# Kernel optimization log

Hardware: AMD Instinct MI355X
Metric: run time of the kernel (lower is better)

## Reference

```python
import jax, jax.numpy as jnp
import numpy as np

N = 50000
E = 600000
IN_DIM = 128
HID = 128
HEADS = 4
OUT = HID // HEADS  # per-head out channels
R = 2
LAYERS = 2
NEG_SLOPE = 0.2


def _glorot(key, shape):
    fan_in, fan_out = shape[-2], shape[-1]
    lim = jnp.sqrt(6.0 / (fan_in + fan_out))
    return jax.random.uniform(key, shape, jnp.float32, -lim, lim)


def setup_inputs() -> dict:
    key = jax.random.key(0)
    ks = jax.random.split(key, 20)
    x = jax.random.normal(ks[0], (N, IN_DIM), jnp.float32)
    eidx = jax.random.randint(ks[1], (2, E), 0, N, jnp.int64 if jax.config.jax_enable_x64 else jnp.int32)
    etype = jax.random.randint(ks[2], (E,), 0, R, eidx.dtype)
    d = IN_DIM
    params = {}
    ki = 3
    for l in range(LAYERS):
        params[f"W{l}"] = _glorot(ks[ki], (R, d, HID)); ki += 1            # per-relation weight
        params[f"Q{l}"] = _glorot(ks[ki], (HID, HEADS)); ki += 1           # query proj (dim=1)
        params[f"K{l}"] = _glorot(ks[ki], (HID, HEADS)); ki += 1           # key proj
        params[f"cb{l}"] = jnp.zeros((HID,), jnp.float32)                   # conv bias
        params[f"pW{l}"] = _glorot(ks[ki], (HID, HID)); ki += 1            # proj Linear weight [out,in]
        params[f"pb{l}"] = jnp.zeros((HID,), jnp.float32)
        d = HID
    return dict(x=x, eidx=eidx, etype=etype, **params)


def _rgat_conv(h, src, dst, etype, W, Q, K, b):
    # per-relation transform of all nodes: [R, N, HID]
    xw = jnp.einsum('ni,rio->rno', h, W)
    out_j = xw[etype, src]          # [E, HID] source features under edge's relation
    out_i = xw[etype, dst]          # [E, HID] target features under edge's relation
    # additive self-attention, dim=1: alpha [E, HEADS]
    alpha = jax.nn.leaky_relu(out_i @ Q + out_j @ K, NEG_SLOPE)
    # segment softmax over destination nodes (across-relation)
    m = jax.ops.segment_max(alpha, dst, num_segments=N)
    m = jnp.where(jnp.isfinite(m), m, 0.0)
    e = jnp.exp(alpha - m[dst])
    s = jax.ops.segment_sum(e, dst, num_segments=N)
    a = e / (s[dst] + 1e-16)
    # weighted messages and scatter-sum aggregation
    msg = out_j.reshape(E, HEADS, OUT) * a[:, :, None]
    agg = jax.ops.segment_sum(msg.reshape(E, HID), dst, num_segments=N)
    return agg + b


def reference(x, eidx, etype, W0, Q0, K0, cb0, pW0, pb0, W1, Q1, K1, cb1, pW1, pb1):
    src, dst = eidx[0], eidx[1]  # flow source_to_target: aggregate at eidx[1]
    h = x
    for (W, Q, K, cb, pW, pb) in ((W0, Q0, K0, cb0, pW0, pb0), (W1, Q1, K1, cb1, pW1, pb1)):
        h = _rgat_conv(h, src, dst, etype, W, Q, K, cb)
        h = jax.nn.elu(h @ pW.T + pb)
    return h
```

## Files before the change

### kernel.cpp

```cpp
#include <hip/hip_runtime.h>
#include <hip/hip_bf16.h>

typedef __hip_bfloat16 bf16;
typedef short s16x8 __attribute__((ext_vector_type(8)));
typedef float f32x4 __attribute__((ext_vector_type(4)));

#define N_NODES 50000
#define NPAD    50048
#define E_EDGES 600000
#define HID     128
#define HEADS   4
#define SCAN_B  196

__device__ __forceinline__ unsigned short f2bf_bits(float f) {
  unsigned u = __float_as_uint(f);
  u += 0x7fffu + ((u >> 16) & 1u);
  return (unsigned short)(u >> 16);
}
__device__ __forceinline__ float bf2f(unsigned short b) {
  return __uint_as_float(((unsigned)b) << 16);
}
__device__ __forceinline__ float lo_f(unsigned v) { return __uint_as_float(v << 16); }
__device__ __forceinline__ float hi_f(unsigned v) { return __uint_as_float(v & 0xffff0000u); }

__device__ __forceinline__ float lrelu(float v) { return fmaxf(v, 0.2f * v); }

__global__ __launch_bounds__(256) void detect_zero_kernel(const unsigned short* __restrict__ xb,
                                                          const int* __restrict__ ei,
                                                          int* __restrict__ flags,
                                                          int* __restrict__ zp, int nz) {
  int t = threadIdx.x;
  int i = blockIdx.x * 256 + t;
  if (i < nz) zp[i] = 0;
  if (blockIdx.x == 0) {
    __shared__ int cnt[2];
    if (t < 2) cnt[t] = 0;
    __syncthreads();
    unsigned short v = xb[2 * t];
    int ex = (v >> 7) & 0xFF;
    if (ex < 119 || ex > 135) atomicAdd(&cnt[0], 1);
    if (ei[2 * t + 1] != 0) atomicAdd(&cnt[1], 1);
    __syncthreads();
    if (t == 0) {
      flags[0] = (cnt[0] > 64) ? 1 : 0;
      flags[1] = (cnt[1] == 0) ? 1 : 0;
    }
  }
}

__global__ __launch_bounds__(256) void cvt_idx_hist_kernel(const int* __restrict__ eidx,
                                                           const int* __restrict__ etype,
                                                           int* __restrict__ dstA, int* __restrict__ pk,
                                                           int* __restrict__ deg,
                                                           const int* __restrict__ flags) {
  int e = blockIdx.x * 256 + threadIdx.x;
  if (e >= E_EDGES) return;
  int s, d, r;
  if (flags[1]) {
    const long long* e64 = (const long long*)eidx;
    const long long* t64 = (const long long*)etype;
    s = (int)e64[e]; d = (int)e64[E_EDGES + e]; r = (int)t64[e];
  } else {
    s = eidx[e]; d = eidx[E_EDGES + e]; r = etype[e];
  }
  dstA[e] = d;
  pk[e] = s | (r << 16);
  atomicAdd(&deg[d], 1);
}

__global__ __launch_bounds__(256) void cvt_xb_kernel(const void* __restrict__ src,
                                                     unsigned short* __restrict__ dst, int n8,
                                                     const int* __restrict__ flags) {
  int i = blockIdx.x * 256 + threadIdx.x;
  if (i >= n8) return;
  if (flags[0]) {
    const float4* s4 = (const float4*)src;
    float4 a = s4[2 * i], b = s4[2 * i + 1];
    s16x8 o;
    o[0] = (short)f2bf_bits(a.x); o[1] = (short)f2bf_bits(a.y);
    o[2] = (short)f2bf_bits(a.z); o[3] = (short)f2bf_bits(a.w);
    o[4] = (short)f2bf_bits(b.x); o[5] = (short)f2bf_bits(b.y);
    o[6] = (short)f2bf_bits(b.z); o[7] = (short)f2bf_bits(b.w);
    *(s16x8*)(dst + (size_t)i * 8) = o;
  } else {
    *(s16x8*)(dst + (size_t)i * 8) = ((const s16x8*)src)[i];
  }
}

__global__ __launch_bounds__(256) void cvt_wt_kernel(const void* __restrict__ src0,
                                                     const void* __restrict__ src1,
                                                     unsigned short* __restrict__ dst,
                                                     const int* __restrict__ flags) {
  int idx = blockIdx.x * 256 + threadIdx.x;
  if (idx >= 2 * 2 * HID * HID) return;
  int l = idx >> 15, rem = idx & 32767;
  int r = rem >> 14, i = (rem >> 7) & 127, o = rem & 127;
  const void* src = l ? src1 : src0;
  unsigned short b;
  if (flags[0]) b = f2bf_bits(((const float*)src)[rem]);
  else          b = ((const unsigned short*)src)[rem];
  dst[(size_t)l * 2 * HID * HID + ((size_t)r * HID + o) * HID + i] = b;
}

struct P8 { const void* src[8]; int dstoff[8]; int n[8]; };
__global__ __launch_bounds__(256) void cvt_params_kernel(P8 tab, float* __restrict__ base,
                                                         const int* __restrict__ flags) {
  const int f = flags[0];
  for (int k = 0; k < 8; ++k) {
    int n = tab.n[k];
    for (int i = blockIdx.x * 256 + threadIdx.x; i < n; i += gridDim.x * 256) {
      float v = f ? ((const float*)tab.src[k])[i] : bf2f(((const unsigned short*)tab.src[k])[i]);
      base[tab.dstoff[k] + i] = v;
    }
  }
}

__global__ __launch_bounds__(256) void scan1_kernel(const int* __restrict__ deg,
                                                    int* __restrict__ excl,
                                                    int* __restrict__ bsum) {
  __shared__ int sm[256];
  int t = threadIdx.x, i = blockIdx.x * 256 + t;
  int v = (i < NPAD) ? deg[i] : 0;
  sm[t] = v;
  __syncthreads();
#pragma unroll
  for (int off = 1; off < 256; off <<= 1) {
    int add = (t >= off) ? sm[t - off] : 0;
    __syncthreads();
    sm[t] += add;
    __syncthreads();
  }
  if (i < NPAD) excl[i] = sm[t] - v;
  if (t == 255) bsum[blockIdx.x] = sm[255];
}

__global__ __launch_bounds__(256) void scan23_kernel(const int* __restrict__ excl,
                                                     const int* __restrict__ bsum,
                                                     int* __restrict__ rowstart) {
  __shared__ int sm[256];
  int t = threadIdx.x;
  int v = (t < SCAN_B) ? bsum[t] : 0;
  sm[t] = v;
  __syncthreads();
#pragma unroll
  for (int off = 1; off < 256; off <<= 1) {
    int add = (t >= off) ? sm[t - off] : 0;
    __syncthreads();
    sm[t] += add;
    __syncthreads();
  }
  int bpre = (blockIdx.x > 0) ? sm[blockIdx.x - 1] : 0;
  int i = blockIdx.x * 256 + t;
  if (i < NPAD) rowstart[i] = excl[i] + bpre;
  if (i == 0) rowstart[NPAD] = E_EDGES;
}

__global__ __launch_bounds__(256) void scatter_kernel(const int* __restrict__ dstA,
                                                      const int* __restrict__ pk,
                                                      const int* __restrict__ rowstart,
                                                      int* __restrict__ cnt,
                                                      int* __restrict__ eord) {
  int e = blockIdx.x * 256 + threadIdx.x;
  if (e >= E_EDGES) return;
  int d = dstA[e];
  int pos = rowstart[d] + atomicAdd(&cnt[d], 1);
  eord[pos] = pk[e];
}


__global__ __launch_bounds__(256) void gemm_xw_mfma(const unsigned short* __restrict__ hb,
                                                    const unsigned short* __restrict__ Wbt,
                                                    unsigned short* __restrict__ xw) {
  __shared__ unsigned short As[64][136];
  const int t = threadIdx.x;
  const int wave = t >> 6, lane = t & 63;
  const int row0 = blockIdx.x * 64;
  const int r = wave >> 1, colb = (wave & 1) * 64;
  const int lm = lane & 15, q = lane >> 4;
  const unsigned short* Bt = Wbt + (size_t)r * HID * HID;
  s16x8 bfr[4][4];
#pragma unroll
  for (int kc = 0; kc < 4; ++kc) {
    const int ko = kc * 32 + q * 8;
#pragma unroll
    for (int ct = 0; ct < 4; ++ct)
      bfr[kc][ct] = *(const s16x8*)(Bt + (size_t)(colb + ct * 16 + lm) * HID + ko);
  }
  const unsigned short* gsrc = hb + (size_t)row0 * HID;
#pragma unroll
  for (int j = 0; j < 4; ++j) {
    int idx = j * 256 + t;
    *(s16x8*)&As[idx >> 4][(idx & 15) * 8] = *(const s16x8*)(gsrc + idx * 8);
  }
  __syncthreads();
  f32x4 acc[4][4];
#pragma unroll
  for (int a = 0; a < 4; ++a)
#pragma unroll
    for (int b = 0; b < 4; ++b) { f32x4 z = {0.f, 0.f, 0.f, 0.f}; acc[a][b] = z; }
#pragma unroll
  for (int kc = 0; kc < 4; ++kc) {
    const int ko = kc * 32 + q * 8;
#pragma unroll
    for (int rt = 0; rt < 4; ++rt) {
      s16x8 a = *(const s16x8*)&As[rt * 16 + lm][ko];
#pragma unroll
      for (int ct = 0; ct < 4; ++ct)
        acc[rt][ct] = __builtin_amdgcn_mfma_f32_16x16x32_bf16(a, bfr[kc][ct], acc[rt][ct], 0, 0, 0);
    }
  }
  __syncthreads();
#pragma unroll
  for (int rr = 0; rr < 2; ++rr) {
    if (r == rr) {
#pragma unroll
      for (int rt = 0; rt < 4; ++rt)
#pragma unroll
        for (int i = 0; i < 4; ++i) {
          int rloc = rt * 16 + q * 4 + i;
#pragma unroll
          for (int ct = 0; ct < 4; ++ct)
            As[rloc][colb + ct * 16 + lm] = f2bf_bits(acc[rt][ct][i]);
        }
    }
    __syncthreads();
    unsigned short* dst = xw + ((size_t)rr * NPAD + row0) * HID;
#pragma unroll
    for (int j = 0; j < 4; ++j) {
      int idx = j * 256 + t;
      int rw = idx >> 4, cb8 = (idx & 15) * 8;
      if (row0 + rw < N_NODES)
        *(s16x8*)(dst + (size_t)rw * HID + cb8) = *(const s16x8*)&As[rw][cb8];
    }
    __syncthreads();
  }
}

__global__ __launch_bounds__(128) void proj_mfma(const unsigned short* __restrict__ aggb,
                                                 const unsigned short* __restrict__ pWTb,
                                                 const float* __restrict__ bo,
                                                 unsigned short* __restrict__ hbout,
                                                 void* __restrict__ dout,
                                                 const int* __restrict__ flags) {
  __shared__ unsigned short As[64][136];
  const int t = threadIdx.x;
  const int wave = t >> 6, lane = t & 63;
  const int row0 = blockIdx.x * 64;
  const int colb = wave * 64;
  const int lm = lane & 15, q = lane >> 4;
  s16x8 bfr[4][4];
#pragma unroll
  for (int kc = 0; kc < 4; ++kc) {
    const int ko = kc * 32 + q * 8;
#pragma unroll
    for (int ct = 0; ct < 4; ++ct)
      bfr[kc][ct] = *(const s16x8*)(pWTb + (size_t)(colb + ct * 16 + lm) * HID + ko);
  }
  const unsigned short* gsrc = aggb + (size_t)row0 * HID;
#pragma unroll
  for (int j = 0; j < 8; ++j) {
    int idx = j * 128 + t;
    *(s16x8*)&As[idx >> 4][(idx & 15) * 8] = *(const s16x8*)(gsrc + idx * 8);
  }
  __syncthreads();
  f32x4 acc[4][4];
#pragma unroll
  for (int a = 0; a < 4; ++a)
#pragma unroll
    for (int b = 0; b < 4; ++b) { f32x4 z = {0.f, 0.f, 0.f, 0.f}; acc[a][b] = z; }
#pragma unroll
  for (int kc = 0; kc < 4; ++kc) {
    const int ko = kc * 32 + q * 8;
#pragma unroll
    for (int rt = 0; rt < 4; ++rt) {
      s16x8 a = *(const s16x8*)&As[rt * 16 + lm][ko];
#pragma unroll
      for (int ct = 0; ct < 4; ++ct)
        acc[rt][ct] = __builtin_amdgcn_mfma_f32_16x16x32_bf16(a, bfr[kc][ct], acc[rt][ct], 0, 0, 0);
    }
  }
  __syncthreads();
  const int f32final = (dout != nullptr) && flags[0];
  if (!f32final) {
    unsigned short* dstp = dout ? (unsigned short*)dout : hbout;
#pragma unroll
    for (int rt = 0; rt < 4; ++rt)
#pragma unroll
      for (int i = 0; i < 4; ++i) {
        int rloc = rt * 16 + q * 4 + i;
#pragma unroll
        for (int ct = 0; ct < 4; ++ct) {
          int o = colb + ct * 16 + lm;
          float v = acc[rt][ct][i] + bo[o];
          v = v > 0.f ? v : expm1f(v);
          As[rloc][o] = f2bf_bits(v);
        }
      }
    __syncthreads();
#pragma unroll
    for (int j = 0; j < 8; ++j) {
      int idx = j * 128 + t;
      int rw = idx >> 4, cb8 = (idx & 15) * 8;
      if (row0 + rw < N_NODES)
        *(s16x8*)(dstp + (size_t)(row0 + rw) * HID + cb8) = *(const s16x8*)&As[rw][cb8];
    }
  } else {
    float* fdst = (float*)dout;
    float (*Fs)[132] = (float(*)[132])&As[0][0];
#pragma unroll
    for (int h = 0; h < 2; ++h) {
#pragma unroll
      for (int rt2 = 0; rt2 < 2; ++rt2) {
        const int rt = h * 2 + rt2;
#pragma unroll
        for (int i = 0; i < 4; ++i) {
          int rloc = rt2 * 16 + q * 4 + i;
#pragma unroll
          for (int ct = 0; ct < 4; ++ct) {
            int o = colb + ct * 16 + lm;
            float v = acc[rt][ct][i] + bo[o];
            v = v > 0.f ? v : expm1f(v);
            Fs[rloc][o] = v;
          }
        }
      }
      __syncthreads();
#pragma unroll
      for (int j = 0; j < 8; ++j) {
        int idx = j * 128 + t;
        int rw = idx >> 5, cb4 = (idx & 31) * 4;
        if (row0 + h * 32 + rw < N_NODES)
          *(float4*)(fdst + (size_t)(row0 + h * 32 + rw) * HID + cb4) = *(const float4*)&Fs[rw][cb4];
      }
      __syncthreads();
    }
  }
}

__global__ __launch_bounds__(256) void prep_wq_kernel(const unsigned short* __restrict__ Wbt,
                                                      const float* __restrict__ Qf,
                                                      const float* __restrict__ Kf,
                                                      unsigned short* __restrict__ qkt_hi,
                                                      unsigned short* __restrict__ qkt_lo) {
  int idx = blockIdx.x * 256 + threadIdx.x;
  if (idx >= 2 * 2 * HID) return;
  int i = idx & 127, lr = idx >> 7, l = lr >> 1, r = (lr & 1);
  float aq[4] = {0.f, 0.f, 0.f, 0.f}, ak[4] = {0.f, 0.f, 0.f, 0.f};
  const unsigned short* Wb = Wbt + (size_t)lr * HID * HID;
  const float* Qp = Qf + l * HID * HEADS;
  const float* Kp = Kf + l * HID * HEADS;
  for (int j = 0; j < HID; ++j) {
    float w = bf2f(Wb[j * HID + i]);
    float4 q4 = *(const float4*)(Qp + j * 4);
    float4 k4 = *(const float4*)(Kp + j * 4);
    aq[0] += w * q4.x; aq[1] += w * q4.y; aq[2] += w * q4.z; aq[3] += w * q4.w;
    ak[0] += w * k4.x; ak[1] += w * k4.y; ak[2] += w * k4.z; ak[3] += w * k4.w;
  }
  size_t base = (size_t)l * 16 * HID;
#pragma unroll
  for (int h = 0; h < 4; ++h) {
    unsigned short qh = f2bf_bits(aq[h]);
    unsigned short kh = f2bf_bits(ak[h]);
    float qres = aq[h] - bf2f(qh);
    float kres = ak[h] - bf2f(kh);
    qkt_hi[base + (size_t)(r * 4 + h) * HID + i] = qh;
    qkt_lo[base + (size_t)(r * 4 + h) * HID + i] = f2bf_bits(qres);
    qkt_hi[base + (size_t)(8 + r * 4 + h) * HID + i] = kh;
    qkt_lo[base + (size_t)(8 + r * 4 + h) * HID + i] = f2bf_bits(kres);
  }
}

__global__ __launch_bounds__(256) void qk_mfma_kernel(const unsigned short* __restrict__ hb,
                                                      const unsigned short* __restrict__ qkt_hi,
                                                      const unsigned short* __restrict__ qkt_lo,
                                                      float4* __restrict__ qi4,
                                                      float4* __restrict__ kj4) {
  __shared__ float st[4][16][68];
  const int wave = threadIdx.x >> 6, lane = threadIdx.x & 63;
  const int row0 = blockIdx.x * 256 + wave * 64;
  const int lm = lane & 15, q = lane >> 4;
  if (row0 < NPAD) {
    s16x8 bhi[4], blo[4], af[4][4];
#pragma unroll
    for (int kc = 0; kc < 4; ++kc) {
      const int ko = kc * 32 + q * 8;
      bhi[kc] = *(const s16x8*)(qkt_hi + (size_t)lm * HID + ko);
      blo[kc] = *(const s16x8*)(qkt_lo + (size_t)lm * HID + ko);
    }
#pragma unroll
    for (int kc = 0; kc < 4; ++kc) {
      const int ko = kc * 32 + q * 8;
#pragma unroll
      for (int rt = 0; rt < 4; ++rt)
        af[kc][rt] = *(const s16x8*)(hb + (size_t)(row0 + rt * 16 + lm) * HID + ko);
    }
    f32x4 acc[4];
#pragma unroll
    for (int a = 0; a < 4; ++a) { f32x4 z = {0.f, 0.f, 0.f, 0.f}; acc[a] = z; }
#pragma unroll
    for (int kc = 0; kc < 4; ++kc)
#pragma unroll
      for (int rt = 0; rt < 4; ++rt) {
        acc[rt] = __builtin_amdgcn_mfma_f32_16x16x32_bf16(af[kc][rt], bhi[kc], acc[rt], 0, 0, 0);
        acc[rt] = __builtin_amdgcn_mfma_f32_16x16x32_bf16(af[kc][rt], blo[kc], acc[rt], 0, 0, 0);
      }
#pragma unroll
    for (int rt = 0; rt < 4; ++rt)
      *(f32x4*)&st[wave][lm][rt * 16 + q * 4] = acc[rt];
  }
  __syncthreads();
  if (row0 < NPAD) {
    int n = row0 + lane;
    if (n < N_NODES) {
      float4 v;
      v.x = st[wave][0][lane]; v.y = st[wave][1][lane]; v.z = st[wave][2][lane]; v.w = st[wave][3][lane];
      qi4[n] = v;
      v.x = st[wave][4][lane]; v.y = st[wave][5][lane]; v.z = st[wave][6][lane]; v.w = st[wave][7][lane];
      qi4[NPAD + n] = v;
      v.x = st[wave][8][lane]; v.y = st[wave][9][lane]; v.z = st[wave][10][lane]; v.w = st[wave][11][lane];
      kj4[n] = v;
      v.x = st[wave][12][lane]; v.y = st[wave][13][lane]; v.z = st[wave][14][lane]; v.w = st[wave][15][lane];
      kj4[NPAD + n] = v;
    }
  }
}

__global__ __launch_bounds__(256) void edge_fused_kernel(
    const int* __restrict__ rowstart, const int* __restrict__ eord,
    const float4* __restrict__ qi4, const float4* __restrict__ kj4,
    const unsigned short* __restrict__ xw, unsigned short* __restrict__ aggb) {
  __shared__ volatile float wls[4][4][72];
  const int wave = threadIdx.x >> 6, lane = threadIdx.x & 63;
  const int n = blockIdx.x * 4 + wave;
  unsigned* outp = (unsigned*)(aggb + ((size_t)n << 7)) + lane;
  const int start = rowstart[n];
  const int deg = rowstart[n + 1] - start;
  if (deg == 0) { *outp = 0u; return; }
  const int hh = lane >> 4;
  const int ch2 = lane << 1;
  float2 acc = {0.f, 0.f};
  float ssel;
  if (deg <= 64) {
    int p = 0;
    float w0 = 0.f, w1 = 0.f, w2 = 0.f, w3 = 0.f;
    if (lane < deg) {
      p = eord[start + lane];
      int s = p & 0xffff, r = p >> 16;
      float4 k4 = kj4[r ? (NPAD + s) : s];
      float4 q4 = r ? qi4[NPAD + n] : qi4[n];
      w0 = __expf(fminf(lrelu(q4.x + k4.x), 85.f));
      w1 = __expf(fminf(lrelu(q4.y + k4.y), 85.f));
      w2 = __expf(fminf(lrelu(q4.z + k4.z), 85.f));
      w3 = __expf(fminf(lrelu(q4.w + k4.w), 85.f));
    }
    float s0 = w0, s1 = w1, s2 = w2, s3 = w3;
#pragma unroll
    for (int off = 32; off > 0; off >>= 1) {
      s0 += __shfl_xor(s0, off); s1 += __shfl_xor(s1, off);
      s2 += __shfl_xor(s2, off); s3 += __shfl_xor(s3, off);
    }
    ssel = hh == 0 ? s0 : hh == 1 ? s1 : hh == 2 ? s2 : s3;
    wls[wave][0][lane] = w0;
    wls[wave][1][lane] = w1;
    wls[wave][2][lane] = w2;
    wls[wave][3][lane] = w3;
    volatile const float* wrh = &wls[wave][hh][0];
    const int degp = (deg + 15) & ~15;
#pragma unroll 1
    for (int e = 0; e < degp; e += 16) {
      int pp[16];
      unsigned vv[16];
#pragma unroll
      for (int u = 0; u < 16; ++u)
        pp[u] = __builtin_amdgcn_readlane(p, e + u);
#pragma unroll
      for (int u = 0; u < 16; ++u)
        vv[u] = *(const unsigned*)(xw + ((size_t)((pp[u] & 0xffff) + (pp[u] >> 16) * NPAD) << 7) + ch2);
#pragma unroll
      for (int u = 0; u < 16; ++u) {
        float we = wrh[e + u];
        acc.x = fmaf(lo_f(vv[u]), we, acc.x);
        acc.y = fmaf(hi_f(vv[u]), we, acc.y);
      }
    }
  } else {
    const float4 q0 = qi4[n], q1 = qi4[NPAD + n];
    float4 m = make_float4(-1e30f, -1e30f, -1e30f, -1e30f);
    for (int e = start; e < start + deg; ++e) {
      int pe = eord[e];
      int s = pe & 0xffff, r = pe >> 16;
      float4 k4 = kj4[(size_t)r * NPAD + s];
      float4 q4 = r ? q1 : q0;
      m.x = fmaxf(m.x, lrelu(q4.x + k4.x)); m.y = fmaxf(m.y, lrelu(q4.y + k4.y));
      m.z = fmaxf(m.z, lrelu(q4.z + k4.z)); m.w = fmaxf(m.w, lrelu(q4.w + k4.w));
    }
    float4 sv = make_float4(0.f, 0.f, 0.f, 0.f);
    for (int e = start; e < start + deg; ++e) {
      int pe = eord[e];
      int s = pe & 0xffff, r = pe >> 16;
      float4 k4 = kj4[(size_t)r * NPAD + s];
      float4 q4 = r ? q1 : q0;
      float w0 = __expf(lrelu(q4.x + k4.x) - m.x);
      float w1 = __expf(lrelu(q4.y + k4.y) - m.y);
      float w2 = __expf(lrelu(q4.z + k4.z) - m.z);
      float w3 = __expf(lrelu(q4.w + k4.w) - m.w);
      sv.x += w0; sv.y += w1; sv.z += w2; sv.w += w3;
      float we = hh == 0 ? w0 : hh == 1 ? w1 : hh == 2 ? w2 : w3;
      unsigned v = *(const unsigned*)(xw + (((size_t)r * NPAD + s) << 7) + ch2);
      acc.x = fmaf(lo_f(v), we, acc.x);
      acc.y = fmaf(hi_f(v), we, acc.y);
    }
    ssel = hh == 0 ? sv.x : hh == 1 ? sv.y : hh == 2 ? sv.z : sv.w;
  }
  float inv = 1.f / (ssel + 1e-16f);
  *outp = (unsigned)f2bf_bits(acc.x * inv) | ((unsigned)f2bf_bits(acc.y * inv) << 16);
}

__global__ __launch_bounds__(64) void prep_proj_kernel(const void* __restrict__ pW0,
                                                       const void* __restrict__ pW1,
                                                       const float* __restrict__ cbf,
                                                       const float* __restrict__ pbf,
                                                       unsigned short* __restrict__ pWTb2,
                                                       float* __restrict__ bo2,
                                                       const int* __restrict__ flags) {
  int o = blockIdx.x & 127, l = blockIdx.x >> 7, t = threadIdx.x;
  const void* pWraw = l ? pW1 : pW0;
  const float* cb = cbf + l * HID;
  const int f = flags[0];
  float part = 0.f;
#pragma unroll
  for (int i = t; i < HID; i += 64) {
    float w = f ? ((const float*)pWraw)[o * HID + i] : bf2f(((const unsigned short*)pWraw)[o * HID + i]);
    pWTb2[(size_t)l * HID * HID + o * HID + i] = f2bf_bits(w);
    part += cb[i] * w;
  }
#pragma unroll
  for (int off = 32; off > 0; off >>= 1) part += __shfl_xor(part, off);
  if (t == 0) bo2[l * HID + o] = pbf[l * HID + o] + part;
}

extern "C" void kernel_launch(void* const* d_in, const int* in_sizes, int n_in,
                              void* d_out, int out_size, void* d_ws, size_t ws_size,
                              hipStream_t stream) {
  const void* x     = d_in[0];
  const int*  eidx  = (const int*)d_in[1];
  const int*  etype = (const int*)d_in[2];
  const int iW[2] = {3, 9}, iQ[2] = {4, 10}, iK[2] = {5, 11}, icb[2] = {6, 12}, ipW[2] = {7, 13}, ipb[2] = {8, 14};

  float* ws = (float*)d_ws;
  size_t off = 0;
  int*   flags = (int*)(ws + off); off += 16;
  unsigned short* hb   = (unsigned short*)(ws + off); off += (size_t)NPAD * HID / 2;
  unsigned short* xw   = (unsigned short*)(ws + off); off += (size_t)NPAD * HID;
  float* qi   = ws + off; off += (size_t)2 * NPAD * HEADS;
  float* kj   = ws + off; off += (size_t)2 * NPAD * HEADS;
  unsigned short* aggb = (unsigned short*)(ws + off); off += (size_t)NPAD * HID / 2;
  int* dstA = (int*)(ws + off); off += E_EDGES;
  int* pk   = (int*)(ws + off); off += E_EDGES;
  int* eord = (int*)(ws + off); off += E_EDGES;
  int* deg  = (int*)(ws + off); off += NPAD;
  int* cnt  = (int*)(ws + off); off += NPAD;
  int* excl = (int*)(ws + off); off += NPAD;
  int* rowstart = (int*)(ws + off); off += NPAD + 16;
  int* bsum  = (int*)(ws + off); off += 256;
  unsigned short* Wbt   = (unsigned short*)(ws + off); off += (size_t)2 * 2 * HID * HID / 2;
  unsigned short* pWTb2 = (unsigned short*)(ws + off); off += (size_t)2 * HID * HID / 2;
  unsigned short* qkt_hi = (unsigned short*)(ws + off); off += (size_t)2 * 16 * HID / 2;
  unsigned short* qkt_lo = (unsigned short*)(ws + off); off += (size_t)2 * 16 * HID / 2;
  float* Qf  = ws + off; off += 2 * HID * HEADS;
  float* Kf  = ws + off; off += 2 * HID * HEADS;
  float* cbf = ws + off; off += 2 * HID;
  float* pbf = ws + off; off += 2 * HID;
  float* bo2 = ws + off; off += 2 * HID;

  detect_zero_kernel<<<(2 * NPAD + 255) / 256, 256, 0, stream>>>((const unsigned short*)x, eidx, flags, deg, 2 * NPAD);
  cvt_idx_hist_kernel<<<(E_EDGES + 255) / 256, 256, 0, stream>>>(eidx, etype, dstA, pk, deg, flags);
  cvt_xb_kernel<<<(N_NODES * HID / 8 + 255) / 256, 256, 0, stream>>>(x, hb, N_NODES * HID / 8, flags);
  cvt_wt_kernel<<<(2 * 2 * HID * HID + 255) / 256, 256, 0, stream>>>(d_in[iW[0]], d_in[iW[1]], Wbt, flags);
  {
    P8 tab;
    float* base = ws;
    for (int l = 0; l < 2; ++l) {
      tab.src[l * 4 + 0] = d_in[iQ[l]];  tab.dstoff[l * 4 + 0] = (int)(Qf - base) + l * HID * HEADS;  tab.n[l * 4 + 0] = HID * HEADS;
      tab.src[l * 4 + 1] = d_in[iK[l]];  tab.dstoff[l * 4 + 1] = (int)(Kf - base) + l * HID * HEADS;  tab.n[l * 4 + 1] = HID * HEADS;
      tab.src[l * 4 + 2] = d_in[icb[l]]; tab.dstoff[l * 4 + 2] = (int)(cbf - base) + l * HID;         tab.n[l * 4 + 2] = HID;
      tab.src[l * 4 + 3] = d_in[ipb[l]]; tab.dstoff[l * 4 + 3] = (int)(pbf - base) + l * HID;         tab.n[l * 4 + 3] = HID;
    }
    cvt_params_kernel<<<2, 256, 0, stream>>>(tab, base, flags);
  }

  scan1_kernel<<<SCAN_B, 256, 0, stream>>>(deg, excl, bsum);
  scan23_kernel<<<SCAN_B, 256, 0, stream>>>(excl, bsum, rowstart);
  scatter_kernel<<<(E_EDGES + 255) / 256, 256, 0, stream>>>(dstA, pk, rowstart, cnt, eord);

  prep_wq_kernel<<<2, 256, 0, stream>>>(Wbt, Qf, Kf, qkt_hi, qkt_lo);
  prep_proj_kernel<<<2 * HID, 64, 0, stream>>>(d_in[ipW[0]], d_in[ipW[1]], cbf, pbf, pWTb2, bo2, flags);

  const int RB = NPAD / 64;
  const int QB = (NPAD + 255) / 256;
  for (int l = 0; l < 2; ++l) {
    gemm_xw_mfma<<<RB, 256, 0, stream>>>(hb, Wbt + (size_t)l * 2 * HID * HID, xw);
    qk_mfma_kernel<<<QB, 256, 0, stream>>>(hb, qkt_hi + (size_t)l * 16 * HID, qkt_lo + (size_t)l * 16 * HID,
                                           (float4*)qi, (float4*)kj);
    edge_fused_kernel<<<N_NODES / 4, 256, 0, stream>>>(rowstart, eord, (const float4*)qi, (const float4*)kj, xw, aggb);
    proj_mfma<<<RB, 128, 0, stream>>>(aggb, pWTb2 + (size_t)l * HID * HID, bo2 + l * HID, hb,
                                      (l == 1) ? d_out : nullptr, flags);
  }
}
```

Baseline: 358.8 us.

## Bucket nodes by degree and process low-degree nodes four per wave

Adds a bucketing pass that splits nodes into low-degree (<=16) and high-degree lists. Low-degree nodes go to a new kernel where each 16-lane quarter-wave handles one node, with 8 channels per lane and a 4-edge unrolled gather. High-degree nodes keep the old per-wave path. With about 12 edges per node on average, this is meant to cut the idle lanes of the one-wave-per-node design. The cost is an extra atomic bucketing kernel, a second edge launch per layer, and a node order that is no longer deterministic.

```diff
diff --git a/kernel.cpp b/kernel.cpp
--- a/kernel.cpp
+++ b/kernel.cpp
@@ -66,6 +66,17 @@
   dstA[e] = d;
   pk[e] = s | (r << 16);
   atomicAdd(&deg[d], 1);
+}
+
+__global__ __launch_bounds__(256) void bucket_kernel(const int* __restrict__ deg,
+                                                     int* __restrict__ bcnt,
+                                                     int* __restrict__ nq,
+                                                     int* __restrict__ nw) {
+  int n = blockIdx.x * 256 + threadIdx.x;
+  if (n >= N_NODES) return;
+  int d = deg[n];
+  if (d <= 16) nq[atomicAdd(&bcnt[0], 1)] = n;
+  else         nw[atomicAdd(&bcnt[1], 1)] = n;
 }
 
 __global__ __launch_bounds__(256) void cvt_xb_kernel(const void* __restrict__ src,
@@ -425,17 +436,95 @@
   }
 }
 
-__global__ __launch_bounds__(256) void edge_fused_kernel(
+__global__ __launch_bounds__(256) void edge_quad_kernel(
     const int* __restrict__ rowstart, const int* __restrict__ eord,
     const float4* __restrict__ qi4, const float4* __restrict__ kj4,
-    const unsigned short* __restrict__ xw, unsigned short* __restrict__ aggb) {
+    const unsigned short* __restrict__ xw, unsigned short* __restrict__ aggb,
+    const int* __restrict__ nq, const int* __restrict__ bcnt) {
+  __shared__ volatile float wls[16][4][17];
+  const int t = threadIdx.x;
+  const int wave = t >> 6, lane = t & 63;
+  const int g = lane >> 4, li = lane & 15;
+  const int idx = blockIdx.x * 16 + wave * 4 + g;
+  const int cq = bcnt[0];
+  const bool act = idx < cq;
+  const int n = act ? nq[idx] : 0;
+  const int start = rowstart[n];
+  const int dg = act ? (rowstart[n + 1] - start) : 0;
+  int p = 0;
+  float w0 = 0.f, w1 = 0.f, w2 = 0.f, w3 = 0.f;
+  if (li < dg) {
+    p = eord[start + li];
+    int s = p & 0xffff, r = p >> 16;
+    float4 k4 = kj4[r ? (NPAD + s) : s];
+    float4 q4 = r ? qi4[NPAD + n] : qi4[n];
+    w0 = __expf(fminf(lrelu(q4.x + k4.x), 85.f));
+    w1 = __expf(fminf(lrelu(q4.y + k4.y), 85.f));
+    w2 = __expf(fminf(lrelu(q4.z + k4.z), 85.f));
+    w3 = __expf(fminf(lrelu(q4.w + k4.w), 85.f));
+  }
+  const int wg = (wave << 2) | g;
+  wls[wg][0][li] = w0; wls[wg][1][li] = w1;
+  wls[wg][2][li] = w2; wls[wg][3][li] = w3;
+  float s0 = w0, s1 = w1, s2 = w2, s3 = w3;
+#pragma unroll
+  for (int off = 8; off > 0; off >>= 1) {
+    s0 += __shfl_xor(s0, off); s1 += __shfl_xor(s1, off);
+    s2 += __shfl_xor(s2, off); s3 += __shfl_xor(s3, off);
+  }
+  const int hh = li >> 2;
+  float ssel = hh == 0 ? s0 : hh == 1 ? s1 : hh == 2 ? s2 : s3;
+  float a0 = 0.f, a1 = 0.f, a2 = 0.f, a3 = 0.f, a4 = 0.f, a5 = 0.f, a6 = 0.f, a7 = 0.f;
+  volatile const float* wrh = &wls[wg][hh][0];
+  const int co = li * 8;
+  const int gbase = lane & 48;
+#pragma unroll 1
+  for (int e0 = 0; e0 < dg; e0 += 4) {
+    int pe[4];
+    uint4 v[4];
+#pragma unroll
+    for (int u = 0; u < 4; ++u) {
+      int e = e0 + u;
+      pe[u] = __shfl(p, gbase + (e < dg ? e : 0));
+    }
+#pragma unroll
+    for (int u = 0; u < 4; ++u)
+      v[u] = *(const uint4*)(xw + ((size_t)((pe[u] & 0xffff) + (pe[u] >> 16) * NPAD) << 7) + co);
+#pragma unroll
+    for (int u = 0; u < 4; ++u) {
+      int e = e0 + u;
+      float we = (e < dg) ? wrh[e] : 0.f;
+      a0 = fmaf(lo_f(v[u].x), we, a0); a1 = fmaf(hi_f(v[u].x), we, a1);
+      a2 = fmaf(lo_f(v[u].y), we, a2); a3 = fmaf(hi_f(v[u].y), we, a3);
+      a4 = fmaf(lo_f(v[u].z), we, a4); a5 = fmaf(hi_f(v[u].z), we, a5);
+      a6 = fmaf(lo_f(v[u].w), we, a6); a7 = fmaf(hi_f(v[u].w), we, a7);
+    }
+  }
+  if (act) {
+    float inv = 1.f / (ssel + 1e-16f);
+    uint4 o;
+    o.x = (unsigned)f2bf_bits(a0 * inv) | ((unsigned)f2bf_bits(a1 * inv) << 16);
+    o.y = (unsigned)f2bf_bits(a2 * inv) | ((unsigned)f2bf_bits(a3 * inv) << 16);
+    o.z = (unsigned)f2bf_bits(a4 * inv) | ((unsigned)f2bf_bits(a5 * inv) << 16);
+    o.w = (unsigned)f2bf_bits(a6 * inv) | ((unsigned)f2bf_bits(a7 * inv) << 16);
+    *(uint4*)(aggb + ((size_t)n << 7) + co) = o;
+  }
+}
+
+__global__ __launch_bounds__(256) void edge_big_kernel(
+    const int* __restrict__ rowstart, const int* __restrict__ eord,
+    const float4* __restrict__ qi4, const float4* __restrict__ kj4,
+    const unsigned short* __restrict__ xw, unsigned short* __restrict__ aggb,
+    const int* __restrict__ nw, const int* __restrict__ bcnt) {
   __shared__ volatile float wls[4][4][72];
   const int wave = threadIdx.x >> 6, lane = threadIdx.x & 63;
-  const int n = blockIdx.x * 4 + wave;
+  const int idx = blockIdx.x * 4 + wave;
+  const int cw = bcnt[1];
+  if (idx >= cw) return;
+  const int n = nw[idx];
   unsigned* outp = (unsigned*)(aggb + ((size_t)n << 7)) + lane;
   const int start = rowstart[n];
   const int deg = rowstart[n + 1] - start;
-  if (deg == 0) { *outp = 0u; return; }
   const int hh = lane >> 4;
   const int ch2 = lane << 1;
   float2 acc = {0.f, 0.f};
@@ -560,9 +649,12 @@
   int* eord = (int*)(ws + off); off += E_EDGES;
   int* deg  = (int*)(ws + off); off += NPAD;
   int* cnt  = (int*)(ws + off); off += NPAD;
+  int* bcnt = (int*)(ws + off); off += 16;
   int* excl = (int*)(ws + off); off += NPAD;
   int* rowstart = (int*)(ws + off); off += NPAD + 16;
   int* bsum  = (int*)(ws + off); off += 256;
+  int* nq   = (int*)(ws + off); off += NPAD;
+  int* nwl  = (int*)(ws + off); off += NPAD;
   unsigned short* Wbt   = (unsigned short*)(ws + off); off += (size_t)2 * 2 * HID * HID / 2;
   unsigned short* pWTb2 = (unsigned short*)(ws + off); off += (size_t)2 * HID * HID / 2;
   unsigned short* qkt_hi = (unsigned short*)(ws + off); off += (size_t)2 * 16 * HID / 2;
@@ -573,8 +665,9 @@
   float* pbf = ws + off; off += 2 * HID;
   float* bo2 = ws + off; off += 2 * HID;
 
-  detect_zero_kernel<<<(2 * NPAD + 255) / 256, 256, 0, stream>>>((const unsigned short*)x, eidx, flags, deg, 2 * NPAD);
+  detect_zero_kernel<<<(2 * NPAD + 16 + 255) / 256, 256, 0, stream>>>((const unsigned short*)x, eidx, flags, deg, 2 * NPAD + 16);
   cvt_idx_hist_kernel<<<(E_EDGES + 255) / 256, 256, 0, stream>>>(eidx, etype, dstA, pk, deg, flags);
+  bucket_kernel<<<(N_NODES + 255) / 256, 256, 0, stream>>>(deg, bcnt, nq, nwl);
   cvt_xb_kernel<<<(N_NODES * HID / 8 + 255) / 256, 256, 0, stream>>>(x, hb, N_NODES * HID / 8, flags);
   cvt_wt_kernel<<<(2 * 2 * HID * HID + 255) / 256, 256, 0, stream>>>(d_in[iW[0]], d_in[iW[1]], Wbt, flags);
   {
@@ -602,7 +695,10 @@
     gemm_xw_mfma<<<RB, 256, 0, stream>>>(hb, Wbt + (size_t)l * 2 * HID * HID, xw);
     qk_mfma_kernel<<<QB, 256, 0, stream>>>(hb, qkt_hi + (size_t)l * 16 * HID, qkt_lo + (size_t)l * 16 * HID,
                                            (float4*)qi, (float4*)kj);
-    edge_fused_kernel<<<N_NODES / 4, 256, 0, stream>>>(rowstart, eord, (const float4*)qi, (const float4*)kj, xw, aggb);
+    edge_quad_kernel<<<(N_NODES + 15) / 16, 256, 0, stream>>>(rowstart, eord, (const float4*)qi, (const float4*)kj,
+                                                              xw, aggb, nq, bcnt);
+    edge_big_kernel<<<(N_NODES + 3) / 4, 256, 0, stream>>>(rowstart, eord, (const float4*)qi, (const float4*)kj,
+                                                           xw, aggb, nwl, bcnt);
     proj_mfma<<<RB, 128, 0, stream>>>(aggb, pWTb2 + (size_t)l * HID * HID, bo2 + l * HID, hb,
                                       (l == 1) ? d_out : nullptr, flags);
   }
```

Result: slower. 872.3 us (+143.1%).
